# Optimization experiments

Hardware: AMD Instinct MI355X
Metric: run time of the kernel (lower is better)

The kernel has to match this reference:

```python
import jax, jax.numpy as jnp
import numpy as np
from itertools import permutations, combinations

BATCH = 32768
EPS = 1e-06  # positivity eps from __init__


def _levi_civita7():
    e = np.zeros((7,) * 7, dtype=np.float32)
    for p in permutations(range(7)):
        inv = sum(1 for i in range(7) for j in range(i + 1, 7) if p[i] > p[j])
        e[p] = -1.0 if inv % 2 else 1.0
    return jnp.asarray(e)

_EPS7 = _levi_civita7()  # (7,7,7,7,7,7,7) rank-7 Levi-Civita tensor
_TRIPLES = np.array(list(combinations(range(7), 3)), dtype=np.int32)  # (35,3) i<j<k index triples
_PERMS3 = [((0, 1, 2), 1.0), ((1, 2, 0), 1.0), ((2, 0, 1), 1.0),
           ((0, 2, 1), -1.0), ((2, 1, 0), -1.0), ((1, 0, 2), -1.0)]


def _phi_full(phi):
    # expand 35 independent components to fully antisymmetric (B,7,7,7)
    b = phi.shape[0]
    pf = jnp.zeros((b, 7, 7, 7), phi.dtype)
    for perm, s in _PERMS3:
        ia = _TRIPLES[:, perm[0]]
        ib = _TRIPLES[:, perm[1]]
        ic = _TRIPLES[:, perm[2]]
        pf = pf.at[:, ia, ib, ic].set(s * phi)
    return pf


def _metric_from_phi(phi):
    # Standard G2 metric: B_ij = (1/144) phi_ikl phi_jmn phi_pqr eps^{klmnpqr};
    # g = B / |det B|^{1/9}  (unit-determinant normalization)
    pf = _phi_full(phi)  # (B,7,7,7)
    C = jnp.einsum('klmnpqr,bpqr->bklmn', _EPS7, pf)  # (B,7,7,7,7)
    T = jnp.einsum('bklmn,bjmn->bklj', C, pf)          # (B,7,7,7)
    Bm = jnp.einsum('bikl,bklj->bij', pf, T) / 144.0   # (B,7,7)
    det = jnp.linalg.det(Bm)
    g = Bm / (jnp.abs(det)[:, None, None] + 1e-12) ** (1.0 / 9.0)
    return 0.5 * (g + jnp.swapaxes(g, -1, -2))  # exact symmetry for eigvalsh


def setup_inputs() -> dict:
    key = jax.random.key(0)
    phi = jax.random.normal(key, (BATCH, 35), dtype=jnp.float32)
    return {"phi": phi}


def reference(phi):
    g = _metric_from_phi(phi)              # (B,7,7)
    ev = jnp.linalg.eigvalsh(g)            # (B,7)
    return jax.nn.relu(-ev + EPS).sum(axis=-1)  # (B,) sum of negative-eigenvalue violations
```

## Files before the change

### kernel.cpp

```cpp
#include <hip/hip_runtime.h>
#include <utility>

#define BATCH 32768
#define NPHI 35

typedef float v2f __attribute__((ext_vector_type(2)));

constexpr int choose2(int n){ return (n*(n-1))/2; }

constexpr int tri_id_sorted(int a,int b,int c){
  int id=0;
  for(int x=0;x<a;++x) id += choose2(6-x);
  for(int y=a+1;y<b;++y) id += (6-y);
  id += (c-b-1);
  return id;
}

constexpr int tri_id3(int a,int b,int c){
  int x=a,y=b,z=c;
  if (x>y){int t=x;x=y;y=t;}
  if (y>z){int t=y;y=z;z=t;}
  if (x>y){int t=x;x=y;y=t;}
  return tri_id_sorted(x,y,z);
}

constexpr int sgn3(int a,int b,int c){
  int inv = (a>b)+(a>c)+(b>c);
  return (inv&1)? -1 : 1;
}

constexpr int UT(int i,int j){
  return i*7 - (i*(i-1))/2 + (j-i);
}

constexpr int PAIR(int k,int l){
  return k*7 - (k*(k+1))/2 + (l - k - 1);
}

struct Prog {
  int n;
  unsigned char kind[1472];
  unsigned char init[1472];
  short         dst [1472];
  unsigned char a   [1472];
  short         b   [1472];
  signed char   s   [1472];
};

constexpr Prog build_prog(){
  Prog P{}; P.n=0;
  bool uinit[28]={};
  for(int k=0;k<7;++k) for(int l=k+1;l<7;++l){
    const int kl = PAIR(k,l);
    bool tinit[7]={};
    for(int m=0;m<7;++m) for(int n2=m+1;n2<7;++n2){
      if(m==k||m==l||n2==k||n2==l) continue;
      int comp[3]={0,0,0}; int cn=0;
      for(int x=0;x<7;++x) if(x!=k&&x!=l&&x!=m&&x!=n2){ comp[cn]=x; ++cn; }
      int perm[7]={k,l,m,n2,comp[0],comp[1],comp[2]};
      int invc=0;
      for(int i=0;i<7;++i) for(int j=i+1;j<7;++j) if(perm[i]>perm[j]) ++invc;
      const int es=(invc&1)? -1 : 1;
      const int tcomp=tri_id_sorted(comp[0],comp[1],comp[2]);
      for(int j=0;j<7;++j){
        if(j==m||j==n2) continue;
        P.kind[P.n]=0;
        P.init[P.n]=tinit[j]?0:1; tinit[j]=true;
        P.dst [P.n]=(short)(kl*7+j);
        P.a   [P.n]=(unsigned char)tcomp;
        P.b   [P.n]=(short)tri_id3(j,m,n2);
        P.s   [P.n]=(signed char)(es*sgn3(j,m,n2));
        ++P.n;
      }
    }
    for(int i=0;i<7;++i){
      if(i==k||i==l) continue;
      for(int j=i;j<7;++j){
        P.kind[P.n]=1;
        P.init[P.n]=uinit[UT(i,j)]?0:1; uinit[UT(i,j)]=true;
        P.dst [P.n]=(short)UT(i,j);
        P.a   [P.n]=(unsigned char)tri_id3(i,k,l);
        P.b   [P.n]=(short)(kl*7+j);
        P.s   [P.n]=(signed char)sgn3(i,k,l);
        ++P.n;
      }
    }
  }
  return P;
}

static constexpr Prog PROG = build_prog();
static_assert(PROG.n == 1470, "program size unexpected");

template<int Q>
__device__ __forceinline__ void step(float (&T)[147], float (&U)[28],
                                     const float (&ph)[NPHI]){
  if constexpr (Q > 0 && PROG.kind[Q] != PROG.kind[Q-1]) {
    __builtin_amdgcn_sched_barrier(0);
  }
  constexpr int  d = PROG.dst[Q];
  constexpr int  a = PROG.a[Q];
  constexpr int  b = PROG.b[Q];
  constexpr bool neg  = (PROG.s[Q] < 0);
  constexpr bool init = (PROG.init[Q] != 0);
  if constexpr (PROG.kind[Q] == 0){
    const float x = neg ? -ph[a] : ph[a];
    if constexpr (init) T[d] = x * ph[b];
    else                T[d] = fmaf(x, ph[b], T[d]);
  } else {
    const float x = neg ? -ph[a] : ph[a];
    if constexpr (init) U[d] = x * T[b];
    else                U[d] = fmaf(x, T[b], U[d]);
  }
}

template<int... Q>
__device__ __forceinline__ void run_prog(float (&T)[147], float (&U)[28],
                                         const float (&ph)[NPHI],
                                         std::integer_sequence<int, Q...>){
  (step<Q>(T, U, ph), ...);
}

#define ROT_BODY(p1, q1, GUARD)                                               \
  {                                                                           \
    const float apq = A[UT(p1,q1)];                                           \
    const float app = A[UT(p1,p1)];                                           \
    const float aqq = A[UT(q1,q1)];                                           \
    bool doit = true;                                                         \
    if (GUARD) doit = __any(fabsf(apq) > 1e-6f*(fabsf(app)+fabsf(aqq)));      \
    if (doit) {                                                               \
      float d = 2.0f*apq;                                                     \
      d = d + ((d >= 0.0f)? 1e-30f : -1e-30f);                                \
      const float tau = (aqq - app) * __builtin_amdgcn_rcpf(d);               \
      float t = __builtin_amdgcn_rcpf(                                        \
                  fabsf(tau) + __builtin_amdgcn_sqrtf(fmaf(tau,tau,1.0f)));   \
      t = (tau >= 0.0f)? t : -t;                                              \
      const float c = __builtin_amdgcn_rsqf(fmaf(t,t,1.0f));                  \
      const float s = t*c;                                                    \
      A[UT(p1,p1)] = fmaf(-t, apq, app);                                      \
      A[UT(q1,q1)] = fmaf( t, apq, aqq);                                      \
      A[UT(p1,q1)] = 0.0f;                                                    \
      const v2f cs  = {  c, s };                                              \
      const v2f msc = { -s, c };                                              \
      _Pragma("unroll")                                                       \
      for (int r=0;r<7;++r){                                                  \
        if (r==p1 || r==q1) continue;                                         \
        const int irp = (r<p1)? UT(r,p1) : UT(p1,r);                          \
        const int irq = (r<q1)? UT(r,q1) : UT(q1,r);                          \
        const v2f arp2 = { A[irp], A[irp] };                                  \
        const v2f arq2 = { A[irq], A[irq] };                                  \
        const v2f res = __builtin_elementwise_fma(cs, arp2, msc*arq2);        \
        A[irp] = res.x;                                                       \
        A[irq] = res.y;                                                       \
      }                                                                       \
    }                                                                         \
  }

__global__ __launch_bounds__(64,1)
void PositivityConstraint_89086211654295_kernel(const float* __restrict__ phi,
                                                float* __restrict__ out){
  const int gid = blockIdx.x*64 + threadIdx.x;

  const float* __restrict__ p = phi + (size_t)gid * NPHI;
  float ph[NPHI];
  {
    const float4* __restrict__ p4 = reinterpret_cast<const float4*>(p);
    #pragma unroll
    for (int k=0;k<8;++k){
      const float4 v = p4[k];
      ph[4*k+0]=v.x; ph[4*k+1]=v.y; ph[4*k+2]=v.z; ph[4*k+3]=v.w;
    }
    ph[32]=p[32]; ph[33]=p[33]; ph[34]=p[34];
  }

  float T[147];
  float U[28];
  run_prog(T, U, ph, std::make_integer_sequence<int, PROG.n>{});
  __builtin_amdgcn_sched_barrier(0);

  float A[28];
  #pragma unroll
  for (int i=0;i<28;++i) A[i] = U[i]*(1.0f/6.0f);

  #pragma unroll 1
  for (int sweep=0; sweep<4; ++sweep){
    #pragma unroll
    for (int p1=0;p1<7;++p1){
      #pragma unroll
      for (int q1=p1+1;q1<7;++q1){
        ROT_BODY(p1, q1, false)
      }
    }
  }
  {
    #pragma unroll
    for (int p1=0;p1<7;++p1){
      #pragma unroll
      for (int q1=p1+1;q1<7;++q1){
        ROT_BODY(p1, q1, true)
      }
    }
  }

  float det = 1.0f;
  #pragma unroll
  for (int i=0;i<7;++i) det *= A[UT(i,i)];
  const float ad = fabsf(det) + 1e-12f;
  const float scale = __builtin_amdgcn_exp2f(__builtin_amdgcn_logf(ad) * (1.0f/9.0f));
  const float inv = __builtin_amdgcn_rcpf(scale);

  float sum = 0.0f;
  #pragma unroll
  for (int i=0;i<7;++i){
    const float ev = A[UT(i,i)]*inv;
    const float r = 1e-6f - ev;
    sum += fmaxf(r, 0.0f);
  }
  out[gid] = sum;
}

extern "C" void kernel_launch(void* const* d_in, const int* in_sizes, int n_in,
                              void* d_out, int out_size, void* d_ws, size_t ws_size,
                              hipStream_t stream) {
  const float* phi = (const float*)d_in[0];
  float* out = (float*)d_out;
  (void)in_sizes; (void)n_in; (void)out_size; (void)d_ws; (void)ws_size;
  hipLaunchKernelGGL(PositivityConstraint_89086211654295_kernel,
                     dim3(BATCH/64), dim3(64), 0, stream, phi, out);
}
```

Baseline: 62.44 us.

## Split metric contraction across four waves per batch tile and reduce via LDS

The 1470-step contraction program is partitioned by (k,l) pair group into four phases. Each of four waves in a 256-thread block runs one phase for the same 64 batch elements, producing partial U accumulators. Waves 1-3 write their partials to shared memory, and wave 0 sums them before doing the Jacobi eigen-solve alone. This raises per-element parallelism when the grid of 512 single-wave blocks underfills the GPU, at the cost of redundant phi loads, an LDS round trip with a block barrier, and three idle waves during the eigen-solve.

```diff
diff --git a/kernel.cpp b/kernel.cpp
--- a/kernel.cpp
+++ b/kernel.cpp
@@ -45,11 +45,11 @@
   unsigned char a   [1472];
   short         b   [1472];
   signed char   s   [1472];
+  unsigned char grp [1472];
 };
 
 constexpr Prog build_prog(){
   Prog P{}; P.n=0;
-  bool uinit[28]={};
   for(int k=0;k<7;++k) for(int l=k+1;l<7;++l){
     const int kl = PAIR(k,l);
     bool tinit[7]={};
@@ -70,6 +70,7 @@
         P.a   [P.n]=(unsigned char)tcomp;
         P.b   [P.n]=(short)tri_id3(j,m,n2);
         P.s   [P.n]=(signed char)(es*sgn3(j,m,n2));
+        P.grp [P.n]=(unsigned char)kl;
         ++P.n;
       }
     }
@@ -77,11 +78,12 @@
       if(i==k||i==l) continue;
       for(int j=i;j<7;++j){
         P.kind[P.n]=1;
-        P.init[P.n]=uinit[UT(i,j)]?0:1; uinit[UT(i,j)]=true;
+        P.init[P.n]=0;
         P.dst [P.n]=(short)UT(i,j);
         P.a   [P.n]=(unsigned char)tri_id3(i,k,l);
         P.b   [P.n]=(short)(kl*7+j);
         P.s   [P.n]=(signed char)sgn3(i,k,l);
+        P.grp [P.n]=(unsigned char)kl;
         ++P.n;
       }
     }
@@ -92,33 +94,38 @@
 static constexpr Prog PROG = build_prog();
 static_assert(PROG.n == 1470, "program size unexpected");
 
-template<int Q>
-__device__ __forceinline__ void step(float (&T)[147], float (&U)[28],
-                                     const float (&ph)[NPHI]){
-  if constexpr (Q > 0 && PROG.kind[Q] != PROG.kind[Q-1]) {
-    __builtin_amdgcn_sched_barrier(0);
-  }
-  constexpr int  d = PROG.dst[Q];
-  constexpr int  a = PROG.a[Q];
-  constexpr int  b = PROG.b[Q];
-  constexpr bool neg  = (PROG.s[Q] < 0);
-  constexpr bool init = (PROG.init[Q] != 0);
-  if constexpr (PROG.kind[Q] == 0){
-    const float x = neg ? -ph[a] : ph[a];
-    if constexpr (init) T[d] = x * ph[b];
-    else                T[d] = fmaf(x, ph[b], T[d]);
-  } else {
-    const float x = neg ? -ph[a] : ph[a];
-    if constexpr (init) U[d] = x * T[b];
-    else                U[d] = fmaf(x, T[b], U[d]);
-  }
-}
-
-template<int... Q>
-__device__ __forceinline__ void run_prog(float (&T)[147], float (&U)[28],
-                                         const float (&ph)[NPHI],
-                                         std::integer_sequence<int, Q...>){
-  (step<Q>(T, U, ph), ...);
+constexpr int PHASE_OF[21] = {
+  3,3,3,3, 0, 1, 3,3, 0, 2, 1, 0, 0, 2, 2, 0, 2, 1, 2, 1, 1
+};
+
+template<int PH, int Q>
+__device__ __forceinline__ void step_if(float (&T)[147], float (&U)[28],
+                                        const float (&ph)[NPHI]){
+  if constexpr (PHASE_OF[PROG.grp[Q]] == PH){
+    if constexpr (Q > 0 && PROG.kind[Q] != PROG.kind[Q-1]) {
+      __builtin_amdgcn_sched_barrier(0);
+    }
+    constexpr int  d = PROG.dst[Q];
+    constexpr int  a = PROG.a[Q];
+    constexpr int  b = PROG.b[Q];
+    constexpr bool neg  = (PROG.s[Q] < 0);
+    constexpr bool init = (PROG.init[Q] != 0);
+    if constexpr (PROG.kind[Q] == 0){
+      const float x = neg ? -ph[a] : ph[a];
+      if constexpr (init) T[d] = x * ph[b];
+      else                T[d] = fmaf(x, ph[b], T[d]);
+    } else {
+      const float x = neg ? -ph[a] : ph[a];
+      U[d] = fmaf(x, T[b], U[d]);
+    }
+  }
+}
+
+template<int PH, int... Q>
+__device__ __forceinline__ void run_phase(float (&T)[147], float (&U)[28],
+                                          const float (&ph)[NPHI],
+                                          std::integer_sequence<int, Q...>){
+  (step_if<PH, Q>(T, U, ph), ...);
 }
 
 #define ROT_BODY(p1, q1, GUARD)                                               \
@@ -156,10 +163,14 @@
     }                                                                         \
   }
 
-__global__ __launch_bounds__(64,1)
+__global__ __launch_bounds__(256,2)
 void PositivityConstraint_89086211654295_kernel(const float* __restrict__ phi,
                                                 float* __restrict__ out){
-  const int gid = blockIdx.x*64 + threadIdx.x;
+  const int wv  = threadIdx.x >> 6;
+  const int ln  = threadIdx.x & 63;
+  const int gid = blockIdx.x*64 + ln;
+
+  __shared__ float Upart[3][64][30];
 
   const float* __restrict__ p = phi + (size_t)gid * NPHI;
   float ph[NPHI];
@@ -175,8 +186,34 @@
 
   float T[147];
   float U[28];
-  run_prog(T, U, ph, std::make_integer_sequence<int, PROG.n>{});
-  __builtin_amdgcn_sched_barrier(0);
+  #pragma unroll
+  for (int i=0;i<28;++i) U[i] = 0.0f;
+
+  switch (wv){
+    case 0: run_phase<0>(T,U,ph, std::make_integer_sequence<int,PROG.n>{}); break;
+    case 1: run_phase<1>(T,U,ph, std::make_integer_sequence<int,PROG.n>{}); break;
+    case 2: run_phase<2>(T,U,ph, std::make_integer_sequence<int,PROG.n>{}); break;
+    default:run_phase<3>(T,U,ph, std::make_integer_sequence<int,PROG.n>{}); break;
+  }
+
+  if (wv){
+    v2f* __restrict__ row = reinterpret_cast<v2f*>(&Upart[wv-1][ln][0]);
+    #pragma unroll
+    for (int k=0;k<14;++k){ v2f t = { U[2*k], U[2*k+1] }; row[k] = t; }
+  }
+  __syncthreads();
+  if (wv) return;
+
+  #pragma unroll
+  for (int h=0;h<3;++h){
+    const v2f* __restrict__ row = reinterpret_cast<const v2f*>(&Upart[h][ln][0]);
+    #pragma unroll
+    for (int k=0;k<14;++k){
+      const v2f t = row[k];
+      U[2*k]   += t.x;
+      U[2*k+1] += t.y;
+    }
+  }
 
   float A[28];
   #pragma unroll
@@ -226,5 +263,5 @@
   float* out = (float*)d_out;
   (void)in_sizes; (void)n_in; (void)out_size; (void)d_ws; (void)ws_size;
   hipLaunchKernelGGL(PositivityConstraint_89086211654295_kernel,
-                     dim3(BATCH/64), dim3(64), 0, stream, phi, out);
-}
+                     dim3(BATCH/64), dim3(256), 0, stream, phi, out);
+}
```

Result: slower. 67.26 us (+7.7%).
